# Kernel optimization log

Measured on AMD Instinct MI355X. Metric: run time of the kernel, lower is better.

The kernel has to match this reference:

```python
import jax, jax.numpy as jnp
import numpy as np

DIRECTIONS = [(0, 0), (1, 0), (-1, 0), (0, 1), (0, -1)]  # (dx, dy)
BN_EPS = 1e-5


def shift2d(x, directions=DIRECTIONS):
    # x: (B, C, H, W). Split channels into G groups, roll each spatially,
    # zero out the wrapped-around border (zero_pad mode), then concat.
    C = x.shape[1]
    G = len(directions)
    base = C // G
    sizes = [base] * (G - 1) + [C - base * (G - 1)]
    starts = np.concatenate([[0], np.cumsum(sizes)])
    out = []
    for i, (dx, dy) in enumerate(directions):
        chunk = x[:, starts[i]:starts[i + 1]]
        if dx == 0 and dy == 0:
            out.append(chunk)
            continue
        y = jnp.roll(chunk, shift=(dy, dx), axis=(-2, -1))
        if dy > 0:
            y = y.at[..., :dy, :].set(0.0)
        elif dy < 0:
            y = y.at[..., dy:, :].set(0.0)
        if dx > 0:
            y = y.at[..., :, :dx].set(0.0)
        elif dx < 0:
            y = y.at[..., :, dx:].set(0.0)
        out.append(y)
    return jnp.concatenate(out, axis=1)


def setup_inputs() -> dict:
    key = jax.random.key(0)
    k1, k2, k3, k4 = jax.random.split(key, 4)
    B, Cin, Cout, H, W = 32, 256, 256, 56, 56
    x = jax.random.normal(k1, (B, Cin, H, W), dtype=jnp.float32)
    pw_w = jax.random.normal(k2, (Cout, Cin), dtype=jnp.float32) * (1.0 / np.sqrt(Cin))
    gamma = jnp.ones((Cout,), dtype=jnp.float32)
    beta = jnp.zeros((Cout,), dtype=jnp.float32)
    running_mean = jax.random.normal(k3, (Cout,), dtype=jnp.float32) * 0.1
    running_var = jax.random.uniform(k4, (Cout,), dtype=jnp.float32, minval=0.5, maxval=1.5)
    return {"x": x, "pw_w": pw_w, "gamma": gamma, "beta": beta,
            "running_mean": running_mean, "running_var": running_var}


def reference(x, pw_w, gamma, beta, running_mean, running_var):
    # Shift (parameter-free spatial mixing)
    y = shift2d(x)
    # stride=1 -> down is Identity
    # 1x1 conv (no bias): pointwise channel mixing
    y = jnp.einsum('bchw,oc->bohw', y, pw_w)
    # BatchNorm2d (inference form with running stats) + ReLU
    inv = gamma * jax.lax.rsqrt(running_var + BN_EPS)
    y = y * inv[None, :, None, None] + (beta - running_mean * inv)[None, :, None, None]
    return jax.nn.relu(y)
```

## Files before the change

kernel.cpp:

```cpp
#include <hip/hip_runtime.h>

#define H_ 56
#define W_ 56
#define HW_ 3136
#define CIN_ 256
#define COUT_ 256

typedef __attribute__((ext_vector_type(8))) short short8;
typedef __attribute__((ext_vector_type(4))) float f32x4;

__device__ unsigned short g_wbf[COUT_ * CIN_];

__device__ __forceinline__ unsigned short f2bf(float f) {
  union { float f; unsigned int i; } v; v.f = f;
  unsigned int b = v.i + (0x7fffu + ((v.i >> 16) & 1u));
  return (unsigned short)(b >> 16);
}

__global__ __launch_bounds__(256)
void prep_weights(const float* __restrict__ wgt) {
  int idx  = blockIdx.x * 256 + threadIdx.x;
  int j    = idx & 7;
  int lane = (idx >> 3) & 63;
  int f    = (idx >> 9) & 3;
  int ks   = (idx >> 11) & 7;
  int wm   = (idx >> 14) & 1;
  int bm   = idx >> 15;
  int m = bm * 128 + wm * 64 + f * 16 + (lane & 15);
  int k = ks * 32 + (lane >> 4) * 8 + j;
  g_wbf[idx] = f2bf(wgt[m * CIN_ + k]);
}

__global__ __launch_bounds__(256, 4)
void shiftconv_gemm(const float* __restrict__ x,
                    const float* __restrict__ gamma,
                    const float* __restrict__ beta,
                    const float* __restrict__ rmean,
                    const float* __restrict__ rvar,
                    float* __restrict__ out)
{
  __shared__ unsigned short Blds[2][64 * 64];
  __shared__ float bnp[256];

  const int t = threadIdx.x;
  const int orig = blockIdx.x;
  const int wgid = (orig & 7) * 392 + (orig >> 3);
  const int bm   = wgid & 1;
  const int bn   = wgid >> 1;

  const int lane = t & 63;
  const int wv   = t >> 6;
  const int wm   = wv >> 1;
  const int wn   = wv & 1;
  const int quad = lane >> 4;
  const int l15  = lane & 15;

  if (t < 128) {
    int o = bm * 128 + t;
    float inv = gamma[o] * rsqrtf(rvar[o] + 1e-5f);
    bnp[2 * t]     = inv;
    bnp[2 * t + 1] = beta[o] - rmean[o] * inv;
  }

  const int nl    = t & 63;
  const int kg    = __builtin_amdgcn_readfirstlane(t >> 6);
  const int kg16  = kg << 4;
  const int nglob = bn * 64 + nl;
  const int bidx  = nglob / HW_;
  const int rem   = nglob - bidx * HW_;
  const int hh    = rem / W_;
  const int ww    = rem - hh * W_;
  const float* __restrict__ px = x + (size_t)bidx * CIN_ * HW_ + hh * W_ + ww;
  const bool mL = (ww >= 1);
  const bool mR = (ww <= W_ - 2);
  const bool mU = (hh >= 1);
  const bool mD = (hh <= H_ - 2);
  const int  h7 = nl & 7;
  unsigned short* const bpA = &Blds[0][nl * 64];
  unsigned short* const bpB = &Blds[1][nl * 64];

  const unsigned short* afrag = g_wbf + (size_t)(bm * 2 + wm) * 16384 + lane * 8;

  f32x4 acc[4][2];
  #pragma unroll
  for (int i = 0; i < 4; ++i)
    #pragma unroll
    for (int j = 0; j < 2; ++j)
      acc[i][j] = (f32x4){0.f, 0.f, 0.f, 0.f};

  float fv[16];

  auto loadB = [&](int kt4) {
    #pragma unroll
    for (int j = 0; j < 16; ++j) {
      int c = kt4 * 64 + kg16 + j;
      int r = (c >= 51) + (c >= 102) + (c >= 153) + (c >= 204);
      int off = (r == 1) ? -1 : (r == 2) ? 1 : (r == 3) ? -W_ :
                (r == 4) ? W_ : 0;
      bool mm = (r == 0) | ((r == 1) & mL) | ((r == 2) & mR) |
                ((r == 3) & mU) | ((r == 4) & mD);
      const float* p = px + (size_t)c * HW_;
      float v = p[mm ? off : 0];
      fv[j] = mm ? v : 0.f;
    }
  };
  auto writeB = [&](unsigned short* bp) {
    unsigned int da[4], db[4];
    #pragma unroll
    for (int j = 0; j < 4; ++j) {
      asm("v_cvt_pk_bf16_f32 %0, %1, %2" : "=v"(da[j]) : "v"(fv[2*j]),     "v"(fv[2*j+1]));
      asm("v_cvt_pk_bf16_f32 %0, %1, %2" : "=v"(db[j]) : "v"(fv[8+2*j]),   "v"(fv[8+2*j+1]));
    }
    int s0 = kg * 2;
    *(uint4*)(bp + (((s0    ) ^ h7) << 3)) = make_uint4(da[0], da[1], da[2], da[3]);
    *(uint4*)(bp + (((s0 | 1) ^ h7) << 3)) = make_uint4(db[0], db[1], db[2], db[3]);
  };

  loadB(0);
  writeB(bpA);
  __syncthreads();

  int buf = 0;

  for (int kt = 0; kt < 4; ++kt) {
    if (kt < 3) loadB(kt + 1);

    #pragma unroll
    for (int ks2 = 0; ks2 < 2; ++ks2) {
      const int kss = kt * 2 + ks2;
      const int sA  = ks2 * 4 + quad;
      short8 af[4], bfr[2];
      #pragma unroll
      for (int f = 0; f < 4; ++f)
        af[f] = *(const short8*)(afrag + kss * 2048 + f * 512);
      #pragma unroll
      for (int g2 = 0; g2 < 2; ++g2) {
        int nl2 = wn * 32 + g2 * 16 + l15;
        bfr[g2] = *(const short8*)(&Blds[buf][nl2 * 64 + ((sA ^ (nl2 & 7)) << 3)]);
      }
      #pragma unroll
      for (int mf = 0; mf < 4; ++mf)
        #pragma unroll
        for (int nf = 0; nf < 2; ++nf)
          acc[mf][nf] = __builtin_amdgcn_mfma_f32_16x16x32_bf16(
              af[mf], bfr[nf], acc[mf][nf], 0, 0, 0);
    }

    if (kt < 3)
      writeB((buf ^ 1) ? bpB : bpA);

    __syncthreads();
    buf ^= 1;
  }

  size_t nbase[2];
  #pragma unroll
  for (int nf = 0; nf < 2; ++nf) {
    int ng  = bn * 64 + wn * 32 + nf * 16 + l15;
    int b2  = ng / HW_;
    int hw2 = ng - b2 * HW_;
    nbase[nf] = (size_t)b2 * COUT_ * HW_ + hw2;
  }
  #pragma unroll
  for (int mf = 0; mf < 4; ++mf) {
    int mloc = wm * 64 + mf * 16 + quad * 4;
    float inv[4], add[4];
    #pragma unroll
    for (int r = 0; r < 4; ++r) {
      inv[r] = bnp[2 * (mloc + r)];
      add[r] = bnp[2 * (mloc + r) + 1];
    }
    size_t obase = (size_t)(bm * 128 + mloc) * HW_;
    #pragma unroll
    for (int nf = 0; nf < 2; ++nf) {
      #pragma unroll
      for (int r = 0; r < 4; ++r) {
        float v = fmaf(acc[mf][nf][r], inv[r], add[r]);
        out[nbase[nf] + obase + (size_t)r * HW_] = fmaxf(v, 0.0f);
      }
    }
  }
}

extern "C" void kernel_launch(void* const* d_in, const int* in_sizes, int n_in,
                              void* d_out, int out_size, void* d_ws, size_t ws_size,
                              hipStream_t stream) {
  const float* x     = (const float*)d_in[0];
  const float* wgt   = (const float*)d_in[1];
  const float* gamma = (const float*)d_in[2];
  const float* beta  = (const float*)d_in[3];
  const float* rmean = (const float*)d_in[4];
  const float* rvar  = (const float*)d_in[5];
  float* out = (float*)d_out;

  prep_weights<<<dim3(256), dim3(256), 0, stream>>>(wgt);
  shiftconv_gemm<<<dim3(3136), dim3(256), 0, stream>>>(x, gamma, beta, rmean, rvar, out);
}
```

Before: 225.8 us.

## Load shifted activations directly into MFMA registers, drop LDS staging, transpose epilogue

Removes the LDS double-buffered B tile and its barriers: each lane now gathers the shifted input values straight into MFMA A-operand registers, and the weights are re-packed so they serve as the B operand with a matching k ordering. Boundary masks and offsets are precomputed per lane, with special cases for the k-groups that straddle shift-group boundaries. The epilogue goes through a padded per-wave LDS transpose so output stores are coalesced along the spatial dimension. The cost is redundant global loads, since each wave reads its own activations without sharing across waves, plus extra registers.

```diff
diff --git a/kernel.cpp b/kernel.cpp
--- a/kernel.cpp
+++ b/kernel.cpp
@@ -22,13 +22,13 @@
   int idx  = blockIdx.x * 256 + threadIdx.x;
   int j    = idx & 7;
   int lane = (idx >> 3) & 63;
-  int f    = (idx >> 9) & 3;
+  int b    = (idx >> 9) & 3;
   int ks   = (idx >> 11) & 7;
-  int wm   = (idx >> 14) & 1;
-  int bm   = idx >> 15;
-  int m = bm * 128 + wm * 64 + f * 16 + (lane & 15);
-  int k = ks * 32 + (lane >> 4) * 8 + j;
-  g_wbf[idx] = f2bf(wgt[m * CIN_ + k]);
+  int wo   = (idx >> 14) & 1;
+  int bo   = idx >> 15;
+  int o = bo * 128 + wo * 64 + b * 16 + (lane & 15);
+  int k = ks * 32 + j * 4 + (lane >> 4);
+  g_wbf[idx] = f2bf(wgt[o * CIN_ + k]);
 }
 
 __global__ __launch_bounds__(256, 4)
@@ -39,146 +39,150 @@
                     const float* __restrict__ rvar,
                     float* __restrict__ out)
 {
-  __shared__ unsigned short Blds[2][64 * 64];
   __shared__ float bnp[256];
+  __shared__ float tbuf[4][32 * 33];
 
   const int t = threadIdx.x;
   const int orig = blockIdx.x;
   const int wgid = (orig & 7) * 392 + (orig >> 3);
-  const int bm   = wgid & 1;
+  const int bo   = wgid & 1;
   const int bn   = wgid >> 1;
 
   const int lane = t & 63;
   const int wv   = t >> 6;
-  const int wm   = wv >> 1;
   const int wn   = wv & 1;
+  const int wo   = wv >> 1;
   const int quad = lane >> 4;
   const int l15  = lane & 15;
 
   if (t < 128) {
-    int o = bm * 128 + t;
+    int o = bo * 128 + t;
     float inv = gamma[o] * rsqrtf(rvar[o] + 1e-5f);
     bnp[2 * t]     = inv;
     bnp[2 * t + 1] = beta[o] - rmean[o] * inv;
   }
-
-  const int nl    = t & 63;
-  const int kg    = __builtin_amdgcn_readfirstlane(t >> 6);
-  const int kg16  = kg << 4;
-  const int nglob = bn * 64 + nl;
-  const int bidx  = nglob / HW_;
-  const int rem   = nglob - bidx * HW_;
-  const int hh    = rem / W_;
-  const int ww    = rem - hh * W_;
-  const float* __restrict__ px = x + (size_t)bidx * CIN_ * HW_ + hh * W_ + ww;
-  const bool mL = (ww >= 1);
-  const bool mR = (ww <= W_ - 2);
-  const bool mU = (hh >= 1);
-  const bool mD = (hh <= H_ - 2);
-  const int  h7 = nl & 7;
-  unsigned short* const bpA = &Blds[0][nl * 64];
-  unsigned short* const bpB = &Blds[1][nl * 64];
-
-  const unsigned short* afrag = g_wbf + (size_t)(bm * 2 + wm) * 16384 + lane * 8;
-
-  f32x4 acc[4][2];
-  #pragma unroll
-  for (int i = 0; i < 4; ++i)
-    #pragma unroll
-    for (int j = 0; j < 2; ++j)
-      acc[i][j] = (f32x4){0.f, 0.f, 0.f, 0.f};
-
-  float fv[16];
-
-  auto loadB = [&](int kt4) {
-    #pragma unroll
-    for (int j = 0; j < 16; ++j) {
-      int c = kt4 * 64 + kg16 + j;
-      int r = (c >= 51) + (c >= 102) + (c >= 153) + (c >= 204);
-      int off = (r == 1) ? -1 : (r == 2) ? 1 : (r == 3) ? -W_ :
-                (r == 4) ? W_ : 0;
-      bool mm = (r == 0) | ((r == 1) & mL) | ((r == 2) & mR) |
-                ((r == 3) & mU) | ((r == 4) & mD);
-      const float* p = px + (size_t)c * HW_;
-      float v = p[mm ? off : 0];
-      fv[j] = mm ? v : 0.f;
-    }
-  };
-  auto writeB = [&](unsigned short* bp) {
-    unsigned int da[4], db[4];
-    #pragma unroll
-    for (int j = 0; j < 4; ++j) {
-      asm("v_cvt_pk_bf16_f32 %0, %1, %2" : "=v"(da[j]) : "v"(fv[2*j]),     "v"(fv[2*j+1]));
-      asm("v_cvt_pk_bf16_f32 %0, %1, %2" : "=v"(db[j]) : "v"(fv[8+2*j]),   "v"(fv[8+2*j+1]));
-    }
-    int s0 = kg * 2;
-    *(uint4*)(bp + (((s0    ) ^ h7) << 3)) = make_uint4(da[0], da[1], da[2], da[3]);
-    *(uint4*)(bp + (((s0 | 1) ^ h7) << 3)) = make_uint4(db[0], db[1], db[2], db[3]);
-  };
-
-  loadB(0);
-  writeB(bpA);
   __syncthreads();
 
-  int buf = 0;
-
-  for (int kt = 0; kt < 4; ++kt) {
-    if (kt < 3) loadB(kt + 1);
-
-    #pragma unroll
-    for (int ks2 = 0; ks2 < 2; ++ks2) {
-      const int kss = kt * 2 + ks2;
-      const int sA  = ks2 * 4 + quad;
-      short8 af[4], bfr[2];
+  const int nglob0 = bn * 64;
+  const int bidx   = nglob0 / HW_;
+  const int rem    = nglob0 - bidx * HW_;
+  const int hw0    = rem + wn * 32 + l15;
+  const int hh0    = hw0 / W_;
+  const int ww0    = hw0 - hh0 * W_;
+  const int hw1    = hw0 + 16;
+  const int hh1    = hw1 / W_;
+  const int ww1    = hw1 - hh1 * W_;
+
+  const int qh = quad * HW_;
+  const unsigned int base0 = (unsigned int)((hw0 + qh) * 4);
+  const unsigned int base1 = (unsigned int)((hw1 + qh) * 4);
+  const bool v0L = (ww0 >= 1),      v1L = (ww1 >= 1);
+  const bool v0R = (ww0 <= W_ - 2), v1R = (ww1 <= W_ - 2);
+  const bool v0U = (hh0 >= 1),      v1U = (hh1 >= 1);
+  const bool v0D = (hh0 <= H_ - 2), v1D = (hh1 <= H_ - 2);
+  unsigned int vo0[5], vo1[5];
+  vo0[0] = base0;                                               vo1[0] = base1;
+  vo0[1] = v0L ? (unsigned int)((hw0 - 1  + qh) * 4) : base0;   vo1[1] = v1L ? (unsigned int)((hw1 - 1  + qh) * 4) : base1;
+  vo0[2] = v0R ? (unsigned int)((hw0 + 1  + qh) * 4) : base0;   vo1[2] = v1R ? (unsigned int)((hw1 + 1  + qh) * 4) : base1;
+  vo0[3] = v0U ? (unsigned int)((hw0 - W_ + qh) * 4) : base0;   vo1[3] = v1U ? (unsigned int)((hw1 - W_ + qh) * 4) : base1;
+  vo0[4] = v0D ? (unsigned int)((hw0 + W_ + qh) * 4) : base0;   vo1[4] = v1D ? (unsigned int)((hw1 + W_ + qh) * 4) : base1;
+  float fm0[5], fm1[5];
+  fm0[0] = 1.f;               fm1[0] = 1.f;
+  fm0[1] = v0L ? 1.f : 0.f;   fm1[1] = v1L ? 1.f : 0.f;
+  fm0[2] = v0R ? 1.f : 0.f;   fm1[2] = v1R ? 1.f : 0.f;
+  fm0[3] = v0U ? 1.f : 0.f;   fm1[3] = v1U ? 1.f : 0.f;
+  fm0[4] = v0D ? 1.f : 0.f;   fm1[4] = v1D ? 1.f : 0.f;
+
+  const char* __restrict__ px = (const char*)(x + (size_t)bidx * CIN_ * HW_);
+  const unsigned short* __restrict__ wp =
+      g_wbf + (size_t)(bo * 2 + wo) * 16384 + lane * 8;
+
+  f32x4 acc[2][4];
+  #pragma unroll
+  for (int a = 0; a < 2; ++a)
+    #pragma unroll
+    for (int b = 0; b < 4; ++b)
+      acc[a][b] = (f32x4){0.f, 0.f, 0.f, 0.f};
+
+  #pragma unroll
+  for (int ks = 0; ks < 8; ++ks) {
+    short8 wf[4];
+    #pragma unroll
+    for (int b = 0; b < 4; ++b)
+      wf[b] = *(const short8*)(wp + ks * 2048 + b * 512);
+
+    float fa0[8], fa1[8];
+    #pragma unroll
+    for (int j = 0; j < 8; ++j) {
+      const int c0 = ks * 32 + 4 * j;
+      unsigned int o0, o1; float m0, m1;
+      if (c0 == 48)       { bool hi = quad >= 3;
+        o0 = hi ? vo0[1] : vo0[0]; o1 = hi ? vo1[1] : vo1[0];
+        m0 = hi ? fm0[1] : 1.f;    m1 = hi ? fm1[1] : 1.f; }
+      else if (c0 == 100) { bool hi = quad >= 2;
+        o0 = hi ? vo0[2] : vo0[1]; o1 = hi ? vo1[2] : vo1[1];
+        m0 = hi ? fm0[2] : fm0[1]; m1 = hi ? fm1[2] : fm1[1]; }
+      else if (c0 == 152) { bool hi = quad >= 1;
+        o0 = hi ? vo0[3] : vo0[2]; o1 = hi ? vo1[3] : vo1[2];
+        m0 = hi ? fm0[3] : fm0[2]; m1 = hi ? fm1[3] : fm1[2]; }
+      else {
+        const int r = (c0 >= 51) + (c0 >= 102) + (c0 >= 153) + (c0 >= 204);
+        o0 = vo0[r]; o1 = vo1[r]; m0 = fm0[r]; m1 = fm1[r];
+      }
+      const unsigned int cb = (unsigned int)(c0 * HW_ * 4);
+      float v0 = *(const float*)(px + (o0 + cb));
+      float v1 = *(const float*)(px + (o1 + cb));
+      fa0[j] = v0 * m0;
+      fa1[j] = v1 * m1;
+    }
+
+    union { short8 v; unsigned int d[4]; } af0, af1;
+    #pragma unroll
+    for (int jj = 0; jj < 4; ++jj) {
+      asm("v_cvt_pk_bf16_f32 %0, %1, %2" : "=v"(af0.d[jj]) : "v"(fa0[2*jj]), "v"(fa0[2*jj+1]));
+      asm("v_cvt_pk_bf16_f32 %0, %1, %2" : "=v"(af1.d[jj]) : "v"(fa1[2*jj]), "v"(fa1[2*jj+1]));
+    }
+
+    #pragma unroll
+    for (int b = 0; b < 4; ++b) {
+      acc[0][b] = __builtin_amdgcn_mfma_f32_16x16x32_bf16(af0.v, wf[b], acc[0][b], 0, 0, 0);
+      acc[1][b] = __builtin_amdgcn_mfma_f32_16x16x32_bf16(af1.v, wf[b], acc[1][b], 0, 0, 0);
+    }
+  }
+
+  float invb[4], addb[4];
+  #pragma unroll
+  for (int b = 0; b < 4; ++b) {
+    int ol = wo * 64 + b * 16 + l15;
+    invb[b] = bnp[2 * ol];
+    addb[b] = bnp[2 * ol + 1];
+  }
+  float* tb = &tbuf[wv][0];
+  const size_t obase0 = (size_t)bidx * COUT_ * HW_;
+  #pragma unroll
+  for (int hb = 0; hb < 2; ++hb) {
+    #pragma unroll
+    for (int bb = 0; bb < 2; ++bb) {
+      const int b = hb * 2 + bb;
       #pragma unroll
-      for (int f = 0; f < 4; ++f)
-        af[f] = *(const short8*)(afrag + kss * 2048 + f * 512);
-      #pragma unroll
-      for (int g2 = 0; g2 < 2; ++g2) {
-        int nl2 = wn * 32 + g2 * 16 + l15;
-        bfr[g2] = *(const short8*)(&Blds[buf][nl2 * 64 + ((sA ^ (nl2 & 7)) << 3)]);
-      }
-      #pragma unroll
-      for (int mf = 0; mf < 4; ++mf)
+      for (int a = 0; a < 2; ++a)
         #pragma unroll
-        for (int nf = 0; nf < 2; ++nf)
-          acc[mf][nf] = __builtin_amdgcn_mfma_f32_16x16x32_bf16(
-              af[mf], bfr[nf], acc[mf][nf], 0, 0, 0);
-    }
-
-    if (kt < 3)
-      writeB((buf ^ 1) ? bpB : bpA);
-
-    __syncthreads();
-    buf ^= 1;
-  }
-
-  size_t nbase[2];
-  #pragma unroll
-  for (int nf = 0; nf < 2; ++nf) {
-    int ng  = bn * 64 + wn * 32 + nf * 16 + l15;
-    int b2  = ng / HW_;
-    int hw2 = ng - b2 * HW_;
-    nbase[nf] = (size_t)b2 * COUT_ * HW_ + hw2;
-  }
-  #pragma unroll
-  for (int mf = 0; mf < 4; ++mf) {
-    int mloc = wm * 64 + mf * 16 + quad * 4;
-    float inv[4], add[4];
-    #pragma unroll
-    for (int r = 0; r < 4; ++r) {
-      inv[r] = bnp[2 * (mloc + r)];
-      add[r] = bnp[2 * (mloc + r) + 1];
-    }
-    size_t obase = (size_t)(bm * 128 + mloc) * HW_;
-    #pragma unroll
-    for (int nf = 0; nf < 2; ++nf) {
-      #pragma unroll
-      for (int r = 0; r < 4; ++r) {
-        float v = fmaf(acc[mf][nf][r], inv[r], add[r]);
-        out[nbase[nf] + obase + (size_t)r * HW_] = fmaxf(v, 0.0f);
-      }
-    }
+        for (int r = 0; r < 4; ++r) {
+          float v = fmaxf(fmaf(acc[a][b][r], invb[b], addb[b]), 0.f);
+          tb[(bb * 16 + l15) * 33 + (a * 16 + quad * 4 + r)] = v;
+        }
+    }
+    asm volatile("s_waitcnt lgkmcnt(0)" ::: "memory");
+    #pragma unroll
+    for (int oi = 0; oi < 16; ++oi) {
+      int ol  = oi * 2 + (lane >> 5);
+      int nl  = lane & 31;
+      float v = tb[ol * 33 + nl];
+      int og  = bo * 128 + wo * 64 + hb * 32 + ol;
+      int hwg = rem + wn * 32 + nl;
+      out[obase0 + (size_t)og * HW_ + hwg] = v;
+    }
+    asm volatile("s_waitcnt lgkmcnt(0)" ::: "memory");
   }
 }
 
```

Result: slower. 231.7 us (+2.6%).
